# Kernel optimization log

Measured on AMD Instinct MI355X. Metric: run time of the kernel, lower is better.

## Reference

```python
import jax, jax.numpy as jnp
import numpy as np

IN_FEATURES = 4096
OUT_FEATURES = 4096
SPARSITY = 0.98


def _build_mask():
    # Mirrors _initialize_structured_sparsity: banded deterministic pattern.
    num_connections = int((1 - SPARSITY) * IN_FEATURES * OUT_FEATURES)
    cpn = max(1, num_connections // OUT_FEATURES)  # connections per neuron (=81)
    rows = np.arange(OUT_FEATURES)[:, None]                      # [O,1]
    cols = (rows * cpn + np.arange(cpn)[None, :]) % IN_FEATURES  # [O,cpn]
    mask = np.zeros((OUT_FEATURES, IN_FEATURES), dtype=np.float32)
    mask[np.repeat(np.arange(OUT_FEATURES), cpn), cols.reshape(-1)] = 1.0
    return mask, cpn


def setup_inputs() -> dict:
    key = jax.random.key(0)
    kx, kw = jax.random.split(key)
    mask_np, cpn = _build_mask()
    x = jax.random.normal(kx, (16384, IN_FEATURES), dtype=jnp.float32)
    # weight init: randn * sqrt(2/cpn) at masked positions (dense tensor is fine;
    # forward multiplies by mask anyway, matching the torch module exactly)
    weight = jax.random.normal(kw, (OUT_FEATURES, IN_FEATURES), dtype=jnp.float32) * jnp.float32(np.sqrt(2.0 / cpn))
    bias = jnp.zeros((OUT_FEATURES,), dtype=jnp.float32)
    mask = jnp.asarray(mask_np)
    return {"x": x, "weight": weight, "bias": bias, "mask": mask}


def reference(x, weight, bias, mask):
    # F.linear(x, weight*mask, bias) == x @ (weight*mask).T + bias
    masked_weight = weight * mask  # [O,I]
    return jnp.einsum('bi,oi->bo', x, masked_weight) + bias
```

## Files before the change

### kernel.cpp

```cpp
#include <hip/hip_runtime.h>
#include <hip/hip_bf16.h>

#define IN_F 4096
#define OUT_F 4096
#define CPN 81
#define OINV 2225
#define OB16 2832

#define BMF 8
#define NCH 16
#define CHUNK 256
#define SC4 84
#define NLD 672
#define XSTR 344
#define RSTRF 8

typedef __attribute__((ext_vector_type(4))) float f32x4;
typedef __attribute__((ext_vector_type(8))) short bf16x8;

__device__ __forceinline__ unsigned short f2bf(float f) {
  __hip_bfloat16 h = __float2bfloat16(f);
  return *reinterpret_cast<unsigned short*>(&h);
}
__device__ __forceinline__ float bf2f(unsigned short u) {
  unsigned int v = ((unsigned int)u) << 16;
  return *reinterpret_cast<float*>(&v);
}

__global__ void prep_wfrag(const float* __restrict__ w,
                           const float* __restrict__ mask,
                           unsigned short* __restrict__ wfrag) {
  int idx = blockIdx.x * 256 + threadIdx.x;
  int lane = idx & 63;
  int t = (idx >> 6) % 3;
  int g = idx / 192;
  int n = lane & 15;
  int kg = lane >> 4;
  int s = g * 16 + n;
  int o = (OINV * s) & 4095;
  unsigned short v8[8];
#pragma unroll
  for (int i = 0; i < 8; ++i) {
    int c = 32 * t + 8 * kg + i;
    int j = c - n;
    float v = 0.f;
    if (j >= 0 && j < CPN) {
      int col = (16 * g + c) & 4095;
      v = w[(size_t)o * IN_F + col] * mask[(size_t)o * IN_F + col];
    }
    v8[i] = f2bf(v);
  }
  *reinterpret_cast<bf16x8*>(wfrag + (size_t)idx * 8) =
      *reinterpret_cast<const bf16x8*>(v8);
}

__global__ __launch_bounds__(512, 4) void sc_fused(
    const float* __restrict__ x, const float* __restrict__ bias,
    const unsigned short* __restrict__ wfrag, float* __restrict__ out) {
  __shared__ unsigned short res[4096 * RSTRF];
  __shared__ unsigned short xl[2][BMF * XSTR];

  const int blk = blockIdx.x;
  const int b0 = blk * BMF;
  const int tid = threadIdx.x;
  const int wave = tid >> 6;
  const int lane = tid & 63;
  const int ln = lane & 15;
  const int lk = lane >> 4;
  const int oln = (OINV * ln) & 4095;
  const int q0 = blk & 15;

  const int i1 = tid + 512;
  const int row0 = tid / SC4, c40 = tid - row0 * SC4;
  const int row1 = i1 / SC4,  c41 = i1 - row1 * SC4;
  const bool v1 = (i1 < NLD);
  const float* xp0 = x + (size_t)(b0 + row0) * IN_F;
  const float* xp1 = x + (size_t)(b0 + row1) * IN_F;
  const int xo0 = row0 * XSTR + 4 * c40;
  const int xo1 = row1 * XSTR + 4 * c41;

  auto loadx = [&](int q, float4& r0, float4& r1) {
    const int c0 = q * CHUNK;
    r0 = *reinterpret_cast<const float4*>(xp0 + ((c0 + 4 * c40) & 4095));
    if (v1) r1 = *reinterpret_cast<const float4*>(xp1 + ((c0 + 4 * c41) & 4095));
  };
  auto drain = [&](int buf, const float4& r0, const float4& r1) {
    ushort4 h;
    h.x = f2bf(r0.x); h.y = f2bf(r0.y); h.z = f2bf(r0.z); h.w = f2bf(r0.w);
    *reinterpret_cast<ushort4*>(&xl[buf][xo0]) = h;
    if (v1) {
      h.x = f2bf(r1.x); h.y = f2bf(r1.y); h.z = f2bf(r1.z); h.w = f2bf(r1.w);
      *reinterpret_cast<ushort4*>(&xl[buf][xo1]) = h;
    }
  };
  auto grp = [&](int g, const unsigned short* ap,
                 bf16x8 b0f, bf16x8 b1f, bf16x8 b2f) {
    bf16x8 a0 = *reinterpret_cast<const bf16x8*>(ap);
    bf16x8 a1 = *reinterpret_cast<const bf16x8*>(ap + 32);
    bf16x8 a2 = *reinterpret_cast<const bf16x8*>(ap + 64);
    f32x4 acc = f32x4{0.f, 0.f, 0.f, 0.f};
    acc = __builtin_amdgcn_mfma_f32_16x16x32_bf16(a0, b0f, acc, 0, 0, 0);
    acc = __builtin_amdgcn_mfma_f32_16x16x32_bf16(a1, b1f, acc, 0, 0, 0);
    acc = __builtin_amdgcn_mfma_f32_16x16x32_bf16(a2, b2f, acc, 0, 0, 0);
    if (lk < 2) {
      int o = (OB16 * g + oln) & 4095;
      ushort4 h;
      h.x = f2bf(acc[0]); h.y = f2bf(acc[1]);
      h.z = f2bf(acc[2]); h.w = f2bf(acc[3]);
      *reinterpret_cast<ushort4*>(res + o * RSTRF + 4 * lk) = h;
    }
  };
  auto compute = [&](int q, int buf) {
    const int gbase = q * 16 + wave * 2;
    const bf16x8* wf = reinterpret_cast<const bf16x8*>(wfrag)
                     + (size_t)gbase * 192 + lane;
    bf16x8 w0 = wf[0],   w1 = wf[64],  w2 = wf[128];
    bf16x8 w3 = wf[192], w4 = wf[256], w5 = wf[320];
    const unsigned short* ap = &xl[buf][(ln & 7) * XSTR + 8 * lk + 32 * wave];
    grp(gbase + 0, ap,      w0, w1, w2);
    grp(gbase + 1, ap + 16, w3, w4, w5);
  };

  float4 A0, A1, B0, B1;
  loadx(q0, A0, A1);
  drain(0, A0, A1);
  loadx((q0 + 1) & 15, B0, B1);
  __syncthreads();

  for (int i = 0; i < NCH; i += 2) {
    const int qa = (q0 + i) & 15;
    const int qb = (q0 + i + 1) & 15;

    if (i + 2 < NCH) loadx((q0 + i + 2) & 15, A0, A1);
    __builtin_amdgcn_sched_barrier(0);
    drain(1, B0, B1);
    compute(qa, 0);
    __syncthreads();

    if (i + 3 < NCH) loadx((q0 + i + 3) & 15, B0, B1);
    __builtin_amdgcn_sched_barrier(0);
    if (i + 2 < NCH) drain(0, A0, A1);
    compute(qb, 1);
    __syncthreads();
  }

  const int j  = lane & 3;
  const int ol = lane >> 2;
#pragma unroll 4
  for (int it = 0; it < 32; ++it) {
    int o = it * 128 + wave * 16 + ol;
    unsigned int v = *reinterpret_cast<const unsigned int*>(res + o * RSTRF + 2 * j);
    float b = bias[o];
    float lo = bf2f((unsigned short)(v & 0xffff)) + b;
    float hi = bf2f((unsigned short)(v >> 16)) + b;
    size_t base = (size_t)(b0 + 2 * j) * OUT_F + o;
    out[base]         = lo;
    out[base + OUT_F] = hi;
  }
}

extern "C" void kernel_launch(void* const* d_in, const int* in_sizes, int n_in,
                              void* d_out, int out_size, void* d_ws, size_t ws_size,
                              hipStream_t stream) {
  const float* x    = (const float*)d_in[0];
  const float* w    = (const float*)d_in[1];
  const float* bias = (const float*)d_in[2];
  const float* mask = (const float*)d_in[3];
  float* out = (float*)d_out;

  unsigned short* wfrag = (unsigned short*)d_ws;

  const int B = in_sizes[0] / IN_F;

  prep_wfrag<<<192, 256, 0, stream>>>(w, mask, wfrag);
  sc_fused<<<B / BMF, 512, 0, stream>>>(x, bias, wfrag, out);
}
```

Baseline: 176.0 us.

## Double batch rows per block to fill MFMA tiles and prefetch weight fragments

Raises the batch tile from 8 to 16 rows with 1024 threads per block, one group per wave. All 16 MFMA rows now carry real data instead of half being wasted on duplicated rows, and each weight fragment is reused across twice as many rows. Weight fragments are now prefetched one chunk ahead in registers, and the epilogue writes four output rows per lane. This needs twice the LDS for the result buffer (128KB) plus a larger x tile, so only one block fits per CU, and 1024-thread blocks may reduce latency hiding.

```diff
diff --git a/kernel.cpp b/kernel.cpp
--- a/kernel.cpp
+++ b/kernel.cpp
@@ -7,13 +7,13 @@
 #define OINV 2225
 #define OB16 2832
 
-#define BMF 8
+#define BMF 16
 #define NCH 16
 #define CHUNK 256
 #define SC4 84
-#define NLD 672
+#define NLD 1344
 #define XSTR 344
-#define RSTRF 8
+#define NTHR 1024
 
 typedef __attribute__((ext_vector_type(4))) float f32x4;
 typedef __attribute__((ext_vector_type(8))) short bf16x8;
@@ -26,6 +26,8 @@
   unsigned int v = ((unsigned int)u) << 16;
   return *reinterpret_cast<float*>(&v);
 }
+
+struct WF3 { bf16x8 w0, w1, w2; };
 
 __global__ void prep_wfrag(const float* __restrict__ w,
                            const float* __restrict__ mask,
@@ -54,10 +56,10 @@
       *reinterpret_cast<const bf16x8*>(v8);
 }
 
-__global__ __launch_bounds__(512, 4) void sc_fused(
+__global__ __launch_bounds__(NTHR, 4) void sc_fused(
     const float* __restrict__ x, const float* __restrict__ bias,
     const unsigned short* __restrict__ wfrag, float* __restrict__ out) {
-  __shared__ unsigned short res[4096 * RSTRF];
+  __shared__ unsigned short res[4096 * BMF];
   __shared__ unsigned short xl[2][BMF * XSTR];
 
   const int blk = blockIdx.x;
@@ -70,14 +72,14 @@
   const int oln = (OINV * ln) & 4095;
   const int q0 = blk & 15;
 
-  const int i1 = tid + 512;
+  const int i1 = tid + NTHR;
   const int row0 = tid / SC4, c40 = tid - row0 * SC4;
   const int row1 = i1 / SC4,  c41 = i1 - row1 * SC4;
   const bool v1 = (i1 < NLD);
   const float* xp0 = x + (size_t)(b0 + row0) * IN_F;
-  const float* xp1 = x + (size_t)(b0 + row1) * IN_F;
+  const float* xp1 = x + (size_t)(b0 + (v1 ? row1 : 0)) * IN_F;
   const int xo0 = row0 * XSTR + 4 * c40;
-  const int xo1 = row1 * XSTR + 4 * c41;
+  const int xo1 = (v1 ? row1 : 0) * XSTR + 4 * (v1 ? c41 : 0);
 
   auto loadx = [&](int q, float4& r0, float4& r1) {
     const int c0 = q * CHUNK;
@@ -93,69 +95,70 @@
       *reinterpret_cast<ushort4*>(&xl[buf][xo1]) = h;
     }
   };
-  auto grp = [&](int g, const unsigned short* ap,
-                 bf16x8 b0f, bf16x8 b1f, bf16x8 b2f) {
+  auto loadwf = [&](int q) -> WF3 {
+    const int g = q * 16 + wave;
+    const bf16x8* wf = reinterpret_cast<const bf16x8*>(wfrag)
+                     + (size_t)g * 192 + lane;
+    WF3 r; r.w0 = wf[0]; r.w1 = wf[64]; r.w2 = wf[128];
+    return r;
+  };
+  auto compute = [&](int q, int buf, const WF3& W) {
+    const int g = q * 16 + wave;
+    const unsigned short* ap = &xl[buf][ln * XSTR + 16 * wave + 8 * lk];
     bf16x8 a0 = *reinterpret_cast<const bf16x8*>(ap);
     bf16x8 a1 = *reinterpret_cast<const bf16x8*>(ap + 32);
     bf16x8 a2 = *reinterpret_cast<const bf16x8*>(ap + 64);
     f32x4 acc = f32x4{0.f, 0.f, 0.f, 0.f};
-    acc = __builtin_amdgcn_mfma_f32_16x16x32_bf16(a0, b0f, acc, 0, 0, 0);
-    acc = __builtin_amdgcn_mfma_f32_16x16x32_bf16(a1, b1f, acc, 0, 0, 0);
-    acc = __builtin_amdgcn_mfma_f32_16x16x32_bf16(a2, b2f, acc, 0, 0, 0);
-    if (lk < 2) {
-      int o = (OB16 * g + oln) & 4095;
-      ushort4 h;
-      h.x = f2bf(acc[0]); h.y = f2bf(acc[1]);
-      h.z = f2bf(acc[2]); h.w = f2bf(acc[3]);
-      *reinterpret_cast<ushort4*>(res + o * RSTRF + 4 * lk) = h;
-    }
-  };
-  auto compute = [&](int q, int buf) {
-    const int gbase = q * 16 + wave * 2;
-    const bf16x8* wf = reinterpret_cast<const bf16x8*>(wfrag)
-                     + (size_t)gbase * 192 + lane;
-    bf16x8 w0 = wf[0],   w1 = wf[64],  w2 = wf[128];
-    bf16x8 w3 = wf[192], w4 = wf[256], w5 = wf[320];
-    const unsigned short* ap = &xl[buf][(ln & 7) * XSTR + 8 * lk + 32 * wave];
-    grp(gbase + 0, ap,      w0, w1, w2);
-    grp(gbase + 1, ap + 16, w3, w4, w5);
+    acc = __builtin_amdgcn_mfma_f32_16x16x32_bf16(a0, W.w0, acc, 0, 0, 0);
+    acc = __builtin_amdgcn_mfma_f32_16x16x32_bf16(a1, W.w1, acc, 0, 0, 0);
+    acc = __builtin_amdgcn_mfma_f32_16x16x32_bf16(a2, W.w2, acc, 0, 0, 0);
+    const int o = (OB16 * g + oln) & 4095;
+    ushort4 h;
+    h.x = f2bf(acc[0]); h.y = f2bf(acc[1]);
+    h.z = f2bf(acc[2]); h.w = f2bf(acc[3]);
+    *reinterpret_cast<ushort4*>(res + o * BMF + 4 * lk) = h;
   };
 
-  float4 A0, A1, B0, B1;
-  loadx(q0, A0, A1);
-  drain(0, A0, A1);
-  loadx((q0 + 1) & 15, B0, B1);
+  float4 xA0, xA1, xB0, xB1;
+  WF3 Wa = loadwf(q0);
+  WF3 Wb = loadwf((q0 + 1) & 15);
+  loadx(q0, xA0, xA1);
+  drain(0, xA0, xA1);
+  loadx((q0 + 1) & 15, xB0, xB1);
   __syncthreads();
 
   for (int i = 0; i < NCH; i += 2) {
     const int qa = (q0 + i) & 15;
     const int qb = (q0 + i + 1) & 15;
 
-    if (i + 2 < NCH) loadx((q0 + i + 2) & 15, A0, A1);
+    if (i + 2 < NCH) loadx((q0 + i + 2) & 15, xA0, xA1);
     __builtin_amdgcn_sched_barrier(0);
-    drain(1, B0, B1);
-    compute(qa, 0);
+    drain(1, xB0, xB1);
+    compute(qa, 0, Wa);
+    if (i + 2 < NCH) Wa = loadwf((q0 + i + 2) & 15);
     __syncthreads();
 
-    if (i + 3 < NCH) loadx((q0 + i + 3) & 15, B0, B1);
+    if (i + 3 < NCH) loadx((q0 + i + 3) & 15, xB0, xB1);
     __builtin_amdgcn_sched_barrier(0);
-    if (i + 2 < NCH) drain(0, A0, A1);
-    compute(qb, 1);
+    if (i + 2 < NCH) drain(0, xA0, xA1);
+    compute(qb, 1, Wb);
+    if (i + 3 < NCH) Wb = loadwf((q0 + i + 3) & 15);
     __syncthreads();
   }
 
-  const int j  = lane & 3;
-  const int ol = lane >> 2;
+  const int ln16 = lane & 15;
+  const int jj = lane >> 4;
 #pragma unroll 4
-  for (int it = 0; it < 32; ++it) {
-    int o = it * 128 + wave * 16 + ol;
-    unsigned int v = *reinterpret_cast<const unsigned int*>(res + o * RSTRF + 2 * j);
+  for (int it = 0; it < 16; ++it) {
+    int o = it * 256 + wave * 16 + ln16;
+    unsigned int v0 = *reinterpret_cast<const unsigned int*>(res + o * BMF + 2 * jj);
+    unsigned int v1 = *reinterpret_cast<const unsigned int*>(res + o * BMF + 8 + 2 * jj);
     float b = bias[o];
-    float lo = bf2f((unsigned short)(v & 0xffff)) + b;
-    float hi = bf2f((unsigned short)(v >> 16)) + b;
-    size_t base = (size_t)(b0 + 2 * j) * OUT_F + o;
-    out[base]         = lo;
-    out[base + OUT_F] = hi;
+    size_t base = (size_t)(b0 + 2 * jj) * OUT_F + o;
+    out[base]                       = bf2f((unsigned short)(v0 & 0xffff)) + b;
+    out[base + OUT_F]               = bf2f((unsigned short)(v0 >> 16)) + b;
+    out[base + 8 * (size_t)OUT_F]   = bf2f((unsigned short)(v1 & 0xffff)) + b;
+    out[base + 9 * (size_t)OUT_F]   = bf2f((unsigned short)(v1 >> 16)) + b;
   }
 }
 
@@ -173,5 +176,5 @@
   const int B = in_sizes[0] / IN_F;
 
   prep_wfrag<<<192, 256, 0, stream>>>(w, mask, wfrag);
-  sc_fused<<<B / BMF, 512, 0, stream>>>(x, bias, wfrag, out);
+  sc_fused<<<B / BMF, NTHR, 0, stream>>>(x, bias, wfrag, out);
 }
```

Measured after the change: 173.9 us. Within noise of the previous version (-1.2%).

## Give each wave a private swizzled x slice and drop per-chunk block barriers

Applied to the files above, without the earlier changes.

Each wave now loads and converts only the x columns its own MFMA groups consume into a wave-private LDS region. The layout is XOR-swizzled and written with 16-byte stores. This removes the two __syncthreads per chunk pair, leaving one barrier before the output epilogue, and the double-buffered shared x tile is gone. The cost is redundant overlap loads, since each wave reads 128 columns where it previously shared a padded tile. Correctness relies on same-wave LDS ordering without an explicit wave barrier.

```diff
diff --git a/kernel.cpp b/kernel.cpp
--- a/kernel.cpp
+++ b/kernel.cpp
@@ -10,13 +10,11 @@
 #define BMF 8
 #define NCH 16
 #define CHUNK 256
-#define SC4 84
-#define NLD 672
-#define XSTR 344
 #define RSTRF 8
 
 typedef __attribute__((ext_vector_type(4))) float f32x4;
 typedef __attribute__((ext_vector_type(8))) short bf16x8;
+typedef __attribute__((ext_vector_type(8))) unsigned short u16x8;
 
 __device__ __forceinline__ unsigned short f2bf(float f) {
   __hip_bfloat16 h = __float2bfloat16(f);
@@ -58,7 +56,7 @@
     const float* __restrict__ x, const float* __restrict__ bias,
     const unsigned short* __restrict__ wfrag, float* __restrict__ out) {
   __shared__ unsigned short res[4096 * RSTRF];
-  __shared__ unsigned short xl[2][BMF * XSTR];
+  __shared__ unsigned short xl[8 * 1024];
 
   const int blk = blockIdx.x;
   const int b0 = blk * BMF;
@@ -67,89 +65,92 @@
   const int lane = tid & 63;
   const int ln = lane & 15;
   const int lk = lane >> 4;
+  const int r8 = lane & 7;
+  const int cq = lane >> 3;
   const int oln = (OINV * ln) & 4095;
   const int q0 = blk & 15;
 
-  const int i1 = tid + 512;
-  const int row0 = tid / SC4, c40 = tid - row0 * SC4;
-  const int row1 = i1 / SC4,  c41 = i1 - row1 * SC4;
-  const bool v1 = (i1 < NLD);
-  const float* xp0 = x + (size_t)(b0 + row0) * IN_F;
-  const float* xp1 = x + (size_t)(b0 + row1) * IN_F;
-  const int xo0 = row0 * XSTR + 4 * c40;
-  const int xo1 = row1 * XSTR + 4 * c41;
+  const int wbase = wave << 10;
+  const float* xrow = x + (size_t)(b0 + r8) * IN_F;
 
-  auto loadx = [&](int q, float4& r0, float4& r1) {
-    const int c0 = q * CHUNK;
-    r0 = *reinterpret_cast<const float4*>(xp0 + ((c0 + 4 * c40) & 4095));
-    if (v1) r1 = *reinterpret_cast<const float4*>(xp1 + ((c0 + 4 * c41) & 4095));
+  auto loadx = [&](int q, float4& p0, float4& p1, float4& p2, float4& p3) {
+    const int cb = q * CHUNK + 32 * wave + 16 * cq;
+    p0 = *reinterpret_cast<const float4*>(xrow + ((cb     ) & 4095));
+    p1 = *reinterpret_cast<const float4*>(xrow + ((cb +  4) & 4095));
+    p2 = *reinterpret_cast<const float4*>(xrow + ((cb +  8) & 4095));
+    p3 = *reinterpret_cast<const float4*>(xrow + ((cb + 12) & 4095));
   };
-  auto drain = [&](int buf, const float4& r0, const float4& r1) {
-    ushort4 h;
-    h.x = f2bf(r0.x); h.y = f2bf(r0.y); h.z = f2bf(r0.z); h.w = f2bf(r0.w);
-    *reinterpret_cast<ushort4*>(&xl[buf][xo0]) = h;
-    if (v1) {
-      h.x = f2bf(r1.x); h.y = f2bf(r1.y); h.z = f2bf(r1.z); h.w = f2bf(r1.w);
-      *reinterpret_cast<ushort4*>(&xl[buf][xo1]) = h;
-    }
+  auto drain = [&](const float4& p0, const float4& p1,
+                   const float4& p2, const float4& p3) {
+    u16x8 h;
+    h[0]=f2bf(p0.x); h[1]=f2bf(p0.y); h[2]=f2bf(p0.z); h[3]=f2bf(p0.w);
+    h[4]=f2bf(p1.x); h[5]=f2bf(p1.y); h[6]=f2bf(p1.z); h[7]=f2bf(p1.w);
+    *reinterpret_cast<u16x8*>(
+        &xl[wbase + (r8 << 7) + ((((2*cq  ) ^ r8) & 15) << 3)]) = h;
+    h[0]=f2bf(p2.x); h[1]=f2bf(p2.y); h[2]=f2bf(p2.z); h[3]=f2bf(p2.w);
+    h[4]=f2bf(p3.x); h[5]=f2bf(p3.y); h[6]=f2bf(p3.z); h[7]=f2bf(p3.w);
+    *reinterpret_cast<u16x8*>(
+        &xl[wbase + (r8 << 7) + ((((2*cq+1) ^ r8) & 15) << 3)]) = h;
   };
-  auto grp = [&](int g, const unsigned short* ap,
-                 bf16x8 b0f, bf16x8 b1f, bf16x8 b2f) {
-    bf16x8 a0 = *reinterpret_cast<const bf16x8*>(ap);
-    bf16x8 a1 = *reinterpret_cast<const bf16x8*>(ap + 32);
-    bf16x8 a2 = *reinterpret_cast<const bf16x8*>(ap + 64);
-    f32x4 acc = f32x4{0.f, 0.f, 0.f, 0.f};
-    acc = __builtin_amdgcn_mfma_f32_16x16x32_bf16(a0, b0f, acc, 0, 0, 0);
-    acc = __builtin_amdgcn_mfma_f32_16x16x32_bf16(a1, b1f, acc, 0, 0, 0);
-    acc = __builtin_amdgcn_mfma_f32_16x16x32_bf16(a2, b2f, acc, 0, 0, 0);
+  auto frag = [&](int j, int t) -> bf16x8 {
+    const int row = ln & 7;
+    const int gr = 2*j + 4*t + lk;
+    return *reinterpret_cast<const bf16x8*>(
+        &xl[wbase + (row << 7) + (((gr ^ row) & 15) << 3)]);
+  };
+  auto scatter = [&](int g, f32x4 acc) {
     if (lk < 2) {
       int o = (OB16 * g + oln) & 4095;
       ushort4 h;
       h.x = f2bf(acc[0]); h.y = f2bf(acc[1]);
       h.z = f2bf(acc[2]); h.w = f2bf(acc[3]);
-      *reinterpret_cast<ushort4*>(res + o * RSTRF + 4 * lk) = h;
+      *reinterpret_cast<ushort4*>(&res[o * RSTRF + 4 * lk]) = h;
     }
   };
-  auto compute = [&](int q, int buf) {
-    const int gbase = q * 16 + wave * 2;
+  auto compute = [&](int q) {
+    const int g0 = q * 16 + 2 * wave;
     const bf16x8* wf = reinterpret_cast<const bf16x8*>(wfrag)
-                     + (size_t)gbase * 192 + lane;
+                     + (size_t)g0 * 192 + lane;
     bf16x8 w0 = wf[0],   w1 = wf[64],  w2 = wf[128];
     bf16x8 w3 = wf[192], w4 = wf[256], w5 = wf[320];
-    const unsigned short* ap = &xl[buf][(ln & 7) * XSTR + 8 * lk + 32 * wave];
-    grp(gbase + 0, ap,      w0, w1, w2);
-    grp(gbase + 1, ap + 16, w3, w4, w5);
+    f32x4 acc = f32x4{0.f, 0.f, 0.f, 0.f};
+    acc = __builtin_amdgcn_mfma_f32_16x16x32_bf16(frag(0,0), w0, acc, 0, 0, 0);
+    acc = __builtin_amdgcn_mfma_f32_16x16x32_bf16(frag(0,1), w1, acc, 0, 0, 0);
+    acc = __builtin_amdgcn_mfma_f32_16x16x32_bf16(frag(0,2), w2, acc, 0, 0, 0);
+    scatter(g0, acc);
+    acc = f32x4{0.f, 0.f, 0.f, 0.f};
+    acc = __builtin_amdgcn_mfma_f32_16x16x32_bf16(frag(1,0), w3, acc, 0, 0, 0);
+    acc = __builtin_amdgcn_mfma_f32_16x16x32_bf16(frag(1,1), w4, acc, 0, 0, 0);
+    acc = __builtin_amdgcn_mfma_f32_16x16x32_bf16(frag(1,2), w5, acc, 0, 0, 0);
+    scatter(g0 + 1, acc);
   };
 
-  float4 A0, A1, B0, B1;
-  loadx(q0, A0, A1);
-  drain(0, A0, A1);
-  loadx((q0 + 1) & 15, B0, B1);
-  __syncthreads();
+  float4 A0, A1, A2, A3, B0, B1, B2, B3;
+  loadx(q0, A0, A1, A2, A3);
 
   for (int i = 0; i < NCH; i += 2) {
     const int qa = (q0 + i) & 15;
     const int qb = (q0 + i + 1) & 15;
 
-    if (i + 2 < NCH) loadx((q0 + i + 2) & 15, A0, A1);
+    loadx(qb, B0, B1, B2, B3);
     __builtin_amdgcn_sched_barrier(0);
-    drain(1, B0, B1);
-    compute(qa, 0);
-    __syncthreads();
+    drain(A0, A1, A2, A3);
+    compute(qa);
 
-    if (i + 3 < NCH) loadx((q0 + i + 3) & 15, B0, B1);
+    if (i + 2 < NCH) loadx((q0 + i + 2) & 15, A0, A1, A2, A3);
     __builtin_amdgcn_sched_barrier(0);
-    if (i + 2 < NCH) drain(0, A0, A1);
-    compute(qb, 1);
-    __syncthreads();
+    drain(B0, B1, B2, B3);
+    compute(qb);
   }
+
+  __syncthreads();
 
   const int j  = lane & 3;
   const int ol = lane >> 2;
 #pragma unroll 4
   for (int it = 0; it < 32; ++it) {
     int o = it * 128 + wave * 16 + ol;
-    unsigned int v = *reinterpret_cast<const unsigned int*>(res + o * RSTRF + 2 * j);
+    unsigned int v = *reinterpret_cast<const unsigned int*>(&res[o * RSTRF + 2 * j]);
     float b = bias[o];
     float lo = bf2f((unsigned short)(v & 0xffff)) + b;
     float hi = bf2f((unsigned short)(v >> 16)) + b;
```

After: 266.7 us. 51.6% more time.
